# Kernel optimization log

Hardware: AMD Instinct MI355X
Metric: run time of the kernel (lower is better)

Reference implementation:

```python
import jax, jax.numpy as jnp
import numpy as np

NEG_MASK = -999.0  # matches masked_fill_(-999) in the torch source

def setup_inputs() -> dict:
    key = jax.random.key(0)
    ks = jax.random.split(key, 8)
    B, N, D = 4, 2048, 768      # batch, nodes, in_dim
    H, Do = 6, 128              # att_head, out_dim (D == H*Do)
    feat_in = jax.random.normal(ks[0], (B, N, D), dtype=jnp.float32)
    adj = jax.random.randint(ks[1], (B, N, N), 0, 2).astype(jnp.int32)
    W = jax.random.normal(ks[2], (H, D, Do), dtype=jnp.float32) * (1.0 / np.sqrt(D))
    b = jnp.zeros((Do,), dtype=jnp.float32)
    w_src = jax.random.normal(ks[3], (H, Do, 1), dtype=jnp.float32) * (1.0 / np.sqrt(Do))
    w_dst = jax.random.normal(ks[4], (H, Do, 1), dtype=jnp.float32) * (1.0 / np.sqrt(Do))
    H_w = jax.random.normal(ks[5], (D, D), dtype=jnp.float32) * (1.0 / np.sqrt(D))
    H_b = jnp.zeros((D,), dtype=jnp.float32)
    return {"feat_in": feat_in, "adj": adj, "W": W, "b": b,
            "w_src": w_src, "w_dst": w_dst, "H_w": H_w, "H_b": H_b}

def reference(feat_in, adj, W, b, w_src, w_dst, H_w, H_b):
    leaky_alpha = 0.2
    B, N, D = feat_in.shape
    Hh = W.shape[0]
    # per-head projection: [B, H, N, Do]
    h = jnp.einsum('bni,hio->bhno', feat_in, W)
    th = jnp.tanh(h)
    attn_src = jnp.einsum('bhno,hoz->bhnz', th, w_src)  # [B,H,N,1]
    attn_dst = jnp.einsum('bhno,hoz->bhnz', th, w_dst)  # [B,H,N,1]
    # additive scores: src_i + dst_j -> [B,H,N,N]
    attn = attn_src + jnp.swapaxes(attn_dst, -1, -2)
    attn = jnp.where(attn >= 0, attn, leaky_alpha * attn)
    mask = (adj == 0)[:, None, :, :]  # [B,1,N,N]
    attn = jnp.where(mask, NEG_MASK, attn)
    attn = jax.nn.softmax(attn, axis=-1)
    feat_out = jnp.einsum('bhnm,bhmo->bhno', attn, h) + b  # [B,H,N,Do]
    feat_out = jnp.swapaxes(feat_out, 1, 2).reshape(B, N, -1)  # [B,N,H*Do]
    feat_out = jax.nn.elu(feat_out)
    gate = jax.nn.sigmoid(feat_in @ H_w.T + H_b)
    out = gate * feat_out + (1.0 - gate) * feat_in
    return out
```

## Files before the change

### kernel.cpp

```cpp
#include <hip/hip_runtime.h>
#include <hip/hip_bf16.h>

#define B_ 4
#define N_ 2048
#define D_ 768
#define H_ 6
#define Do_ 128
#define M_ (B_*N_)
#define C2_ (2*D_)
#define SROW 49152

typedef __attribute__((ext_vector_type(8))) short bf16x8;
typedef __attribute__((ext_vector_type(4))) float f32x4;
typedef __attribute__((ext_vector_type(4))) int int4v;
typedef __attribute__((ext_vector_type(2))) int int2v;
typedef __attribute__((ext_vector_type(4))) float float4v;
typedef __attribute__((ext_vector_type(4))) unsigned short ushort4v;

__device__ __forceinline__ float b2f(short s){
    unsigned u = ((unsigned)(unsigned short)s) << 16;
    return __builtin_bit_cast(float, u);
}
__device__ __forceinline__ short f2b(float f){
    unsigned u = __builtin_bit_cast(unsigned, f);
    unsigned r = (u + 0x7fffu + ((u >> 16) & 1u)) >> 16;
    return (short)r;
}
__device__ __forceinline__ int pk2(float a, float b){
    unsigned ua = __builtin_bit_cast(unsigned, a) + 0x8000u;
    unsigned ub = __builtin_bit_cast(unsigned, b) + 0x8000u;
    return (int)__builtin_amdgcn_perm(ub, ua, 0x07060302u);
}
__device__ __forceinline__ float fast_tanh(float x){
    float a = fabsf(x);
    float e = __expf(-2.0f * a);
    float t = (1.0f - e) / (1.0f + e);
    return copysignf(t, x);
}
__device__ __forceinline__ void gload_lds16(const void* g, void* l){
    __builtin_amdgcn_global_load_lds((const __attribute__((address_space(1))) unsigned int*)g,
                                     (__attribute__((address_space(3))) unsigned int*)l,
                                     16, 0, 0);
}

#define HT_IDX(bh, n, o) ((((size_t)((bh)*64 + ((n) >> 5))*128 + (o))*32) + ((n) & 31))

__global__ __launch_bounds__(256) void k_prep_pack(const float* __restrict__ W,
                                                   const float* __restrict__ Hw,
                                                   const int* __restrict__ adj,
                                                   short* __restrict__ bmat,
                                                   unsigned char* __restrict__ pk){
    __shared__ short Ts[128][136];
    int bid = blockIdx.x, t = threadIdx.x;
    if (bid < 36){
        int hd = bid / 6, kc = bid % 6, k0 = kc * 128;
        const float* wb = W + (size_t)hd*D_*Do_ + (size_t)k0*Do_;
        #pragma unroll
        for (int i = 0; i < 16; i++){
            int u = t + i*256;
            int krow = u >> 5, o4 = (u & 31) * 4;
            float4v v = *(const float4v*)&wb[krow*Do_ + o4];
            #pragma unroll
            for (int e = 0; e < 4; e++) Ts[o4 + e][krow] = f2b(v[e]);
        }
        __syncthreads();
        #pragma unroll
        for (int i = 0; i < 8; i++){
            int u = t + i*256;
            int orow = u >> 4, cu = (u & 15) * 8;
            *(int4v*)&bmat[(size_t)(hd*128 + orow)*D_ + k0 + cu] = *(const int4v*)&Ts[orow][cu];
        }
    } else if (bid < 36 + D_){
        int d = bid - 36;
        const float* hp = Hw + (size_t)d*D_;
        for (int k = t; k < D_; k += 256) bmat[(size_t)(D_ + d)*D_ + k] = f2b(hp[k]);
    } else {
        int g = (bid - 36 - D_)*256 + t;
        const int* ap = adj + (size_t)g*8;
        int4v a0 = *(const int4v*)ap;
        int4v a1 = *(const int4v*)(ap + 4);
        unsigned by = 0;
        #pragma unroll
        for (int i = 0; i < 4; i++){
            by |= (a0[i] ? 1u : 0u) << i;
            by |= (a1[i] ? 1u : 0u) << (i + 4);
        }
        pk[g] = (unsigned char)by;
    }
}

__global__ __launch_bounds__(256) void k_gemm(const float* __restrict__ A,
                                              const short* __restrict__ Bm,
                                              short* __restrict__ ht,
                                              float* outg){
    __shared__ short As[128][72];
    __shared__ short Bs[128*64];
    int tid = threadIdx.x;
    int mBase = blockIdx.y * 128, cBase = blockIdx.x * 128;
    int wave = tid >> 6, lane = tid & 63, q = lane >> 4, nL = lane & 15;
    int wr = (wave >> 1) * 64, wc = (wave & 1) * 64;
    int srow = tid >> 3;
    int sc16 = (tid & 7) ^ (srow & 7);
    const short* bSrc = Bm + (size_t)(cBase + srow)*D_ + sc16*8;
    short* bDst = &Bs[wave*512];
    f32x4 acc[4][4] = {};
    for (int kk = 0; kk < D_; kk += 64){
        __syncthreads();
        #pragma unroll
        for (int i = 0; i < 4; i++)
            gload_lds16(bSrc + (size_t)i*32*D_ + kk, bDst + i*2048);
        #pragma unroll
        for (int i = 0; i < 8; i++){
            int idx = tid + i*256;
            int row = idx >> 4, c4 = (idx & 15) * 4;
            float4v av = *(const float4v*)&A[(mBase+row)*D_ + kk + c4];
            int2v w; w[0] = pk2(av[0], av[1]); w[1] = pk2(av[2], av[3]);
            *(int2v*)&As[row][c4] = w;
        }
        __syncthreads();
        #pragma unroll
        for (int k2 = 0; k2 < 64; k2 += 32){
            bf16x8 aF[4], bF[4];
            int cb = (k2 >> 3) + q;
            #pragma unroll
            for (int rt = 0; rt < 4; rt++) aF[rt] = *(const bf16x8*)&As[wr + rt*16 + nL][k2 + q*8];
            #pragma unroll
            for (int ct = 0; ct < 4; ct++){
                int r = wc + ct*16 + nL;
                bF[ct] = *(const bf16x8*)&Bs[r*64 + ((cb ^ (r & 7)) * 8)];
            }
            #pragma unroll
            for (int rt = 0; rt < 4; rt++)
                #pragma unroll
                for (int ct = 0; ct < 4; ct++)
                    acc[rt][ct] = __builtin_amdgcn_mfma_f32_16x16x32_bf16(aF[rt], bF[ct], acc[rt][ct], 0, 0, 0);
        }
    }
    if (cBase < D_){
        int hd = cBase >> 7;
        #pragma unroll
        for (int rt = 0; rt < 4; rt++){
            #pragma unroll
            for (int ct = 0; ct < 4; ct++){
                int o  = (wc + ct*16 + nL) & 127;
                int m0 = mBase + wr + rt*16 + q*4;
                int b = m0 >> 11, n0 = m0 & 2047;
                int bh = b*H_ + hd;
                ushort4v v;
                #pragma unroll
                for (int r = 0; r < 4; r++) v[r] = (unsigned short)f2b(acc[rt][ct][r]);
                *(ushort4v*)&ht[HT_IDX(bh, n0, o)] = v;
            }
        }
    } else {
        #pragma unroll
        for (int rt = 0; rt < 4; rt++){
            #pragma unroll
            for (int ct = 0; ct < 4; ct++){
                int d  = cBase - D_ + wc + ct*16 + nL;
                int m0 = mBase + wr + rt*16 + q*4;
                #pragma unroll
                for (int r = 0; r < 4; r++) outg[(size_t)(m0 + r)*D_ + d] = acc[rt][ct][r];
            }
        }
    }
}

__global__ __launch_bounds__(256) void k_stats(const short* __restrict__ ht,
                                               const float* __restrict__ wsrc,
                                               const float* __restrict__ wdst,
                                               float* __restrict__ srcP,
                                               float* __restrict__ dstP){
    int g = blockIdx.x * 256 + threadIdx.x;
    int y = blockIdx.y, o0 = y * 32;
    int bh = g >> 11, n = g & 2047;
    int hd = bh % H_;
    const short* hp = ht + HT_IDX(bh, n, o0);
    const float* ws = wsrc + hd*Do_ + o0;
    const float* wd = wdst + hd*Do_ + o0;
    float as = 0.f, ad = 0.f;
    for (int o = 0; o < 32; o++){
        float t = fast_tanh(b2f(hp[o*32]));
        as += t * ws[o];
        ad += t * wd[o];
    }
    srcP[y*SROW + g] = as; dstP[y*SROW + g] = ad;
}

struct StageS {
    float E1[2048];
    float E2[2048];
    unsigned pkw[64*65];
};
struct RedS { float red[2][64][37]; };
union LdsU { StageS s; RedS r; };

#define PV_EPILOGUE(ACC, ACCL, FOFF)                                          \
    {                                                                         \
        _Pragma("unroll")                                                     \
        for (int r = 0; r < 4; r++){                                          \
            int i = r0 + rh*32 + (FOFF) + q*4 + r;                            \
            float invl = 1.0f / (ACCL)[r];                                    \
            size_t baseO = (size_t)(b*N_ + i)*D_ + hd*Do_;                    \
            _Pragma("unroll")                                                 \
            for (int ct = 0; ct < 8; ct++){                                   \
                int o = ct*16 + nL;                                           \
                float v = (ACC)[ct][r]*invl + bias[o];                        \
                float e = v > 0.f ? v : __expf(v) - 1.0f;                     \
                float gl = outg[baseO + o] + Hb[hd*Do_ + o];                  \
                float g = 1.0f / (1.0f + __expf(-gl));                        \
                float fi = feat_in[baseO + o];                                \
                outg[baseO + o] = g*e + (1.0f - g)*fi;                        \
            }                                                                 \
        }                                                                     \
    }

__global__ __launch_bounds__(256) void k_pv(const unsigned char* __restrict__ pkG,
                                            const float* __restrict__ srcP,
                                            const float* __restrict__ dstP,
                                            const short* __restrict__ ht,
                                            const float* __restrict__ feat_in,
                                            const float* __restrict__ bias,
                                            const float* __restrict__ Hb,
                                            float* outg){
    __shared__ LdsU U;
    int lid = blockIdx.x;
    int nid = (lid & 7)*96 + (lid >> 3);
    int itile = nid & 31;
    int hd = (nid >> 5) % 6, b = nid / 192;
    int tid = threadIdx.x, wave = tid >> 6, lane = tid & 63, q = lane >> 4, nL = lane & 15;
    int rh = wave >> 1, kh = wave & 1;
    int r0 = itile * 64;
    int bh = b*H_ + hd;
    {
        const float4v* g0 = (const float4v*)(dstP + bh*N_);
        const float4v* g1 = (const float4v*)(dstP + SROW + bh*N_);
        const float4v* g2 = (const float4v*)(dstP + 2*SROW + bh*N_);
        const float4v* g3 = (const float4v*)(dstP + 3*SROW + bh*N_);
        #pragma unroll
        for (int h = 0; h < 2; h++){
            int c4 = tid*2 + h;
            float4v d = g0[c4] + g1[c4] + g2[c4] + g3[c4];
            #pragma unroll
            for (int t = 0; t < 4; t++){
                U.s.E1[c4*4 + t] = __expf(d[t]);
                U.s.E2[c4*4 + t] = __expf(0.2f * d[t]);
            }
        }
        const unsigned* pg = (const unsigned*)(pkG + (size_t)(b*N_ + r0) * (N_/8));
        #pragma unroll
        for (int k = 0; k < 16; k++){
            int idx = tid + k*256;
            U.s.pkw[(idx >> 6)*65 + (idx & 63)] = pg[idx];
        }
    }
    __syncthreads();
    int rowL0 = rh*32 + nL, rowL1 = rowL0 + 16;
    int gi0 = bh*N_ + r0 + rowL0, gi1 = bh*N_ + r0 + rowL1;
    float s0 = srcP[gi0] + srcP[SROW+gi0] + srcP[2*SROW+gi0] + srcP[3*SROW+gi0];
    float s1 = srcP[gi1] + srcP[SROW+gi1] + srcP[2*SROW+gi1] + srcP[3*SROW+gi1];
    float e1r0 = __expf(s0), e2r0 = __expf(0.2f*s0);
    float e1r1 = __expf(s1), e2r1 = __expf(0.2f*s1);
    bf16x8 vone;
    #pragma unroll
    for (int t = 0; t < 8; t++) vone[t] = (short)0x3F80;
    const short* hp = ht + (size_t)bh*262144;
    f32x4 acc[2][8] = {};
    f32x4 accl0 = {}, accl1 = {};
    int base0 = rowL0*65, base1 = rowL1*65;
    int jEnd = kh*1024 + 1024;
    for (int j0 = kh*1024; j0 < jEnd; j0 += 32){
        unsigned by0 = (U.s.pkw[base0 + (j0 >> 5)] >> (q*8)) & 0xFF;
        unsigned by1 = (U.s.pkw[base1 + (j0 >> 5)] >> (q*8)) & 0xFF;
        int kb = j0 + q*8;
        const short* hj = hp + (size_t)(j0 >> 5)*4096 + q*8;
        float4v E1a = *(const float4v*)&U.s.E1[kb];
        float4v E1b = *(const float4v*)&U.s.E1[kb + 4];
        float4v E2a = *(const float4v*)&U.s.E2[kb];
        float4v E2b = *(const float4v*)&U.s.E2[kb + 4];
        float p0[8], p1[8];
        #pragma unroll
        for (int t = 0; t < 8; t++){
            float E1t = t < 4 ? E1a[t] : E1b[t-4];
            float E2t = t < 4 ? E2a[t] : E2b[t-4];
            float a0 = fmaxf(e1r0*E1t, e2r0*E2t);
            float a1 = fmaxf(e1r1*E1t, e2r1*E2t);
            p0[t] = ((by0 >> t) & 1u) ? a0 : 0.0f;
            p1[t] = ((by1 >> t) & 1u) ? a1 : 0.0f;
        }
        int4v pi0, pi1;
        #pragma unroll
        for (int tp = 0; tp < 4; tp++){
            pi0[tp] = pk2(p0[2*tp], p0[2*tp+1]);
            pi1[tp] = pk2(p1[2*tp], p1[2*tp+1]);
        }
        bf16x8 pf0 = __builtin_bit_cast(bf16x8, pi0);
        bf16x8 pf1 = __builtin_bit_cast(bf16x8, pi1);
        #pragma unroll
        for (int ct = 0; ct < 8; ct++){
            bf16x8 bF = *(const bf16x8*)&hj[(ct*16 + nL)*32];
            acc[0][ct] = __builtin_amdgcn_mfma_f32_16x16x32_bf16(pf0, bF, acc[0][ct], 0, 0, 0);
            acc[1][ct] = __builtin_amdgcn_mfma_f32_16x16x32_bf16(pf1, bF, acc[1][ct], 0, 0, 0);
        }
        accl0 = __builtin_amdgcn_mfma_f32_16x16x32_bf16(pf0, vone, accl0, 0, 0, 0);
        accl1 = __builtin_amdgcn_mfma_f32_16x16x32_bf16(pf1, vone, accl1, 0, 0, 0);
    }
    __syncthreads();
    if (kh == 1){
        #pragma unroll
        for (int ct = 0; ct < 8; ct++)
            #pragma unroll
            for (int r = 0; r < 4; r++) U.r.red[rh][lane][ct*4 + r] = acc[0][ct][r];
        #pragma unroll
        for (int r = 0; r < 4; r++) U.r.red[rh][lane][32 + r] = accl0[r];
    }
    __syncthreads();
    if (kh == 0){
        #pragma unroll
        for (int ct = 0; ct < 8; ct++)
            #pragma unroll
            for (int r = 0; r < 4; r++) acc[0][ct][r] += U.r.red[rh][lane][ct*4 + r];
        #pragma unroll
        for (int r = 0; r < 4; r++) accl0[r] += U.r.red[rh][lane][32 + r];
    }
    __syncthreads();
    if (kh == 0){
        #pragma unroll
        for (int ct = 0; ct < 8; ct++)
            #pragma unroll
            for (int r = 0; r < 4; r++) U.r.red[rh][lane][ct*4 + r] = acc[1][ct][r];
        #pragma unroll
        for (int r = 0; r < 4; r++) U.r.red[rh][lane][32 + r] = accl1[r];
    }
    __syncthreads();
    if (kh == 1){
        #pragma unroll
        for (int ct = 0; ct < 8; ct++)
            #pragma unroll
            for (int r = 0; r < 4; r++) acc[1][ct][r] += U.r.red[rh][lane][ct*4 + r];
        #pragma unroll
        for (int r = 0; r < 4; r++) accl1[r] += U.r.red[rh][lane][32 + r];
    }
    if (kh == 0){
        PV_EPILOGUE(acc[0], accl0, 0)
    } else {
        PV_EPILOGUE(acc[1], accl1, 16)
    }
}

extern "C" void kernel_launch(void* const* d_in, const int* in_sizes, int n_in,
                              void* d_out, int out_size, void* d_ws, size_t ws_size,
                              hipStream_t stream){
    const float* feat = (const float*)d_in[0];
    const int*   adj  = (const int*)  d_in[1];
    const float* W    = (const float*)d_in[2];
    const float* bias = (const float*)d_in[3];
    const float* wsrc = (const float*)d_in[4];
    const float* wdst = (const float*)d_in[5];
    const float* Hw   = (const float*)d_in[6];
    const float* Hb   = (const float*)d_in[7];
    float* out = (float*)d_out;
    char* ws = (char*)d_ws;
    short* bmat = (short*)(ws);
    short* ht   = (short*)(ws + 2359296);
    float* srcP = (float*)(ws + 14942208);
    float* dstP = (float*)(ws + 15728640);
    unsigned char* pk = (unsigned char*)(ws + 16515072);

    hipLaunchKernelGGL(k_prep_pack, dim3(36 + D_ + 8192), dim3(256), 0, stream, W, Hw, adj, bmat, pk);
    hipLaunchKernelGGL(k_gemm,      dim3(12, 64),     dim3(256), 0, stream, feat, bmat, ht, out);
    hipLaunchKernelGGL(k_stats,     dim3(192, 4),     dim3(256), 0, stream, ht, wsrc, wdst, srcP, dstP);
    hipLaunchKernelGGL(k_pv,        dim3(768),        dim3(256), 0, stream, pk, srcP, dstP,
                       ht, feat, bias, Hb, out);
}
```

Measured before the change: 268.8 us.

## Double-buffer value tiles into LDS via async global-to-LDS loads in PV loop

The PV kernel previously read the bf16 value (h) tiles straight from global memory for every MFMA B operand. Now waves with rh==0 prefetch the next 4096-element tile into a double-buffered LDS region with gload_lds16, and all waves read B fragments from LDS. Because waves rh=0 and rh=1 read the same tiles, the redundant global traffic goes away. This adds a __syncthreads every iteration and 32KB more LDS, which may lower occupancy. The mask select is also rewritten as an sbfe-based bitwise AND.

```diff
diff --git a/kernel.cpp b/kernel.cpp
--- a/kernel.cpp
+++ b/kernel.cpp
@@ -187,13 +187,14 @@
     srcP[y*SROW + g] = as; dstP[y*SROW + g] = ad;
 }
 
-struct StageS {
+struct LoopS {
     float E1[2048];
     float E2[2048];
     unsigned pkw[64*65];
+    short bft[2][2][4096];
 };
 struct RedS { float red[2][64][37]; };
-union LdsU { StageS s; RedS r; };
+union LdsU { LoopS s; RedS r; };
 
 #define PV_EPILOGUE(ACC, ACCL, FOFF)                                          \
     {                                                                         \
@@ -232,6 +233,7 @@
     int rh = wave >> 1, kh = wave & 1;
     int r0 = itile * 64;
     int bh = b*H_ + hd;
+    const short* hp = ht + (size_t)bh*262144;
     {
         const float4v* g0 = (const float4v*)(dstP + bh*N_);
         const float4v* g1 = (const float4v*)(dstP + SROW + bh*N_);
@@ -252,6 +254,12 @@
         for (int k = 0; k < 16; k++){
             int idx = tid + k*256;
             U.s.pkw[(idx >> 6)*65 + (idx & 63)] = pg[idx];
+        }
+        if (rh == 0){
+            const short* s0 = hp + (size_t)(kh*32)*4096 + lane*8;
+            #pragma unroll
+            for (int i = 0; i < 8; i++)
+                gload_lds16(s0 + i*512, &U.s.bft[kh][0][i*512]);
         }
     }
     __syncthreads();
@@ -264,29 +272,37 @@
     bf16x8 vone;
     #pragma unroll
     for (int t = 0; t < 8; t++) vone[t] = (short)0x3F80;
-    const short* hp = ht + (size_t)bh*262144;
     f32x4 acc[2][8] = {};
     f32x4 accl0 = {}, accl1 = {};
     int base0 = rowL0*65, base1 = rowL1*65;
-    int jEnd = kh*1024 + 1024;
-    for (int j0 = kh*1024; j0 < jEnd; j0 += 32){
-        unsigned by0 = (U.s.pkw[base0 + (j0 >> 5)] >> (q*8)) & 0xFF;
-        unsigned by1 = (U.s.pkw[base1 + (j0 >> 5)] >> (q*8)) & 0xFF;
-        int kb = j0 + q*8;
-        const short* hj = hp + (size_t)(j0 >> 5)*4096 + q*8;
+    int p = 0;
+    for (int t = 0; t < 32; t++){
+        int jt = kh*32 + t;
+        if (t < 31 && rh == 0){
+            const short* sn = hp + (size_t)(jt + 1)*4096 + lane*8;
+            short* dn = &U.s.bft[kh][p^1][0];
+            #pragma unroll
+            for (int i = 0; i < 8; i++)
+                gload_lds16(sn + i*512, dn + i*512);
+        }
+        unsigned by0 = (U.s.pkw[base0 + jt] >> (q*8)) & 0xFF;
+        unsigned by1 = (U.s.pkw[base1 + jt] >> (q*8)) & 0xFF;
+        int kb = jt*32 + q*8;
         float4v E1a = *(const float4v*)&U.s.E1[kb];
         float4v E1b = *(const float4v*)&U.s.E1[kb + 4];
         float4v E2a = *(const float4v*)&U.s.E2[kb];
         float4v E2b = *(const float4v*)&U.s.E2[kb + 4];
         float p0[8], p1[8];
         #pragma unroll
-        for (int t = 0; t < 8; t++){
-            float E1t = t < 4 ? E1a[t] : E1b[t-4];
-            float E2t = t < 4 ? E2a[t] : E2b[t-4];
+        for (int t8 = 0; t8 < 8; t8++){
+            float E1t = t8 < 4 ? E1a[t8] : E1b[t8-4];
+            float E2t = t8 < 4 ? E2a[t8] : E2b[t8-4];
             float a0 = fmaxf(e1r0*E1t, e2r0*E2t);
             float a1 = fmaxf(e1r1*E1t, e2r1*E2t);
-            p0[t] = ((by0 >> t) & 1u) ? a0 : 0.0f;
-            p1[t] = ((by1 >> t) & 1u) ? a1 : 0.0f;
+            int m0 = __builtin_amdgcn_sbfe((int)by0, t8, 1);
+            int m1 = __builtin_amdgcn_sbfe((int)by1, t8, 1);
+            p0[t8] = __builtin_bit_cast(float, __builtin_bit_cast(int, a0) & m0);
+            p1[t8] = __builtin_bit_cast(float, __builtin_bit_cast(int, a1) & m1);
         }
         int4v pi0, pi1;
         #pragma unroll
@@ -296,16 +312,18 @@
         }
         bf16x8 pf0 = __builtin_bit_cast(bf16x8, pi0);
         bf16x8 pf1 = __builtin_bit_cast(bf16x8, pi1);
+        const short* bt = &U.s.bft[kh][p][q*8];
         #pragma unroll
         for (int ct = 0; ct < 8; ct++){
-            bf16x8 bF = *(const bf16x8*)&hj[(ct*16 + nL)*32];
+            bf16x8 bF = *(const bf16x8*)&bt[(ct*16 + nL)*32];
             acc[0][ct] = __builtin_amdgcn_mfma_f32_16x16x32_bf16(pf0, bF, acc[0][ct], 0, 0, 0);
             acc[1][ct] = __builtin_amdgcn_mfma_f32_16x16x32_bf16(pf1, bF, acc[1][ct], 0, 0, 0);
         }
         accl0 = __builtin_amdgcn_mfma_f32_16x16x32_bf16(pf0, vone, accl0, 0, 0, 0);
         accl1 = __builtin_amdgcn_mfma_f32_16x16x32_bf16(pf1, vone, accl1, 0, 0, 0);
-    }
-    __syncthreads();
+        __syncthreads();
+        p ^= 1;
+    }
     if (kh == 1){
         #pragma unroll
         for (int ct = 0; ct < 8; ct++)
```

After: 269.5 us. No clear change (+0.3%).
